# Optimization experiments

Measured on AMD Instinct MI355X. Metric: run time of the kernel, lower is better.

The kernel has to match this reference:

```python
import jax, jax.numpy as jnp
import numpy as np
import math

B, S, D, H, FF = 4, 1024, 1024, 16, 4096
DK = D // H
EPS = 1e-6


def _gelu(x):
    return 0.5 * x * (1 + jnp.tanh(math.sqrt(2 / math.pi) * (x + 0.044715 * x ** 3)))


def _layernorm(x, g, b):
    # torch LayerNorm clone: unbiased std, divide by (std + eps)
    mean = jnp.mean(x, axis=-1, keepdims=True)
    var = jnp.sum((x - mean) ** 2, axis=-1, keepdims=True) / (x.shape[-1] - 1)
    std = jnp.sqrt(var)
    return g * (x - mean) / (std + EPS) + b


def setup_inputs() -> dict:
    key = jax.random.key(0)
    ks = jax.random.split(key, 16)
    sc_d = 1.0 / math.sqrt(D)
    sc_ff = 1.0 / math.sqrt(FF)
    inp = {
        "query": jax.random.normal(ks[0], (B, S, D), jnp.float32),
        "key": jax.random.normal(ks[1], (B, S, D), jnp.float32),
        "value": jax.random.normal(ks[2], (B, S, D), jnp.float32),
        "mask": jnp.ones((B, S), jnp.int32),
        "Wq": jax.random.normal(ks[3], (D, D), jnp.float32) * sc_d,
        "bq": jnp.zeros((D,), jnp.float32),
        "Wk": jax.random.normal(ks[4], (D, D), jnp.float32) * sc_d,
        "bk": jnp.zeros((D,), jnp.float32),
        "Wv": jax.random.normal(ks[5], (D, D), jnp.float32) * sc_d,
        "bv": jnp.zeros((D,), jnp.float32),
        "Wo": jax.random.normal(ks[6], (D, D), jnp.float32) * sc_d,
        "bo": jnp.zeros((D,), jnp.float32),
        "W1": jax.random.normal(ks[7], (FF, D), jnp.float32) * sc_d,
        "b1": jnp.zeros((FF,), jnp.float32),
        "W2": jax.random.normal(ks[8], (D, FF), jnp.float32) * sc_ff,
        "b2": jnp.zeros((D,), jnp.float32),
        "g1": jnp.ones((D,), jnp.float32),
        "be1": jnp.zeros((D,), jnp.float32),
        "g2": jnp.ones((D,), jnp.float32),
        "be2": jnp.zeros((D,), jnp.float32),
    }
    return inp


def reference(query, key, value, mask, Wq, bq, Wk, bk, Wv, bv, Wo, bo,
              W1, b1, W2, b2, g1, be1, g2, be2):
    # self-attention: q = k = v = query (with_external=False)
    def proj(x, W, b):
        return (x @ W.T + b).reshape(B, S, H, DK).transpose(0, 2, 1, 3)  # [B,H,S,DK]

    q = proj(query, Wq, bq)
    k = proj(query, Wk, bk)
    v = proj(query, Wv, bv)
    scores = jnp.einsum("bhqd,bhkd->bhqk", q, k) / math.sqrt(DK)
    # 2D mask [B,S] broadcasts as [B,1,1,S] over key positions
    scores = jnp.where(mask[:, None, None, :] == 0, -1e9, scores)
    p = jax.nn.softmax(scores, axis=-1)
    attn = jnp.einsum("bhqk,bhkd->bhqd", p, v)
    attn = attn.transpose(0, 2, 1, 3).reshape(B, S, D)
    x = attn @ Wo.T + bo
    x = _layernorm(query + x, g1, be1)
    residual = x
    h1 = x @ W1.T + b1
    x2 = _gelu(h1 @ W2.T + b2)  # note: gelu applied AFTER fc2, per source
    return _layernorm(residual + x2, g2, be2)
```

## Files before the change

### kernel.cpp

```cpp
#include <hip/hip_runtime.h>
#include <hip/hip_bf16.h>
#include <math.h>

typedef __bf16 bf16;
typedef __bf16 bf16x8 __attribute__((ext_vector_type(8)));
typedef float floatx4 __attribute__((ext_vector_type(4)));

#define NT 4096
#define DMODEL 1024
#define NHEAD 16
#define DHEAD 64
#define FFDIM 4096

__device__ __forceinline__ void load_lds16(const void* g, void* l) {
    __builtin_amdgcn_global_load_lds(
        (const __attribute__((address_space(1))) void*)g,
        (__attribute__((address_space(3))) void*)l,
        16, 0, 0);
}

__device__ __forceinline__ unsigned short f2bf(float f) {
    bf16 h = (bf16)f;
    return __builtin_bit_cast(unsigned short, h);
}

__device__ __forceinline__ float gelu_f(float v) {
    return 0.5f * v * (1.0f + tanhf(0.7978845608028654f * (v + 0.044715f * v * v * v)));
}

__global__ __launch_bounds__(256) void cast_kernel(
    const float* __restrict__ q, const float* __restrict__ wq, const float* __restrict__ wk,
    const float* __restrict__ wv, const float* __restrict__ wo, const float* __restrict__ w1,
    const float* __restrict__ w2, const float* __restrict__ bq, const float* __restrict__ bk,
    const float* __restrict__ bv, bf16* __restrict__ xbf, bf16* __restrict__ wqkv,
    bf16* __restrict__ wob, bf16* __restrict__ w1b, bf16* __restrict__ w2b,
    float* __restrict__ bqkv)
{
    int gid = blockIdx.x * 256 + threadIdx.x;
    if (gid < 3072)
        bqkv[gid] = gid < 1024 ? bq[gid] : (gid < 2048 ? bk[gid - 1024] : bv[gid - 2048]);

    const float4* src;
    ushort4* dst;
    int off = gid;
    if (off < 1048576)                  { src = (const float4*)q;  dst = (ushort4*)xbf; }
    else if ((off -= 1048576) < 262144) { src = (const float4*)wq; dst = (ushort4*)wqkv; }
    else if ((off -= 262144) < 262144)  { src = (const float4*)wk; dst = (ushort4*)wqkv + 262144; }
    else if ((off -= 262144) < 262144)  { src = (const float4*)wv; dst = (ushort4*)wqkv + 524288; }
    else if ((off -= 262144) < 262144)  { src = (const float4*)wo; dst = (ushort4*)wob; }
    else if ((off -= 262144) < 1048576) { src = (const float4*)w1; dst = (ushort4*)w1b; }
    else { off -= 1048576;                src = (const float4*)w2; dst = (ushort4*)w2b; }

    float4 v = src[off];
    ushort4 u;
    u.x = f2bf(v.x); u.y = f2bf(v.y); u.z = f2bf(v.z); u.w = f2bf(v.w);
    dst[off] = u;
}

template <int EPI, int TN, int SPLITK = 1>
__global__ __launch_bounds__(256) void gemm_bt(
    const bf16* __restrict__ A, const bf16* __restrict__ Wt,
    const float* __restrict__ bias, const float* __restrict__ res,
    void* __restrict__ outp, int M, int N, int K)
{
    constexpr int NJ = TN / 32;
    __shared__ __align__(16) bf16 As[128 * 64];
    __shared__ __align__(16) bf16 Bs[TN * 64];

    const int t = threadIdx.x;
    const int lane = t & 63, wave = t >> 6;
    const int l15 = lane & 15, quad = lane >> 4;
    const int wm = wave & 1, wn = wave >> 1;
    const int m0 = blockIdx.x * 128, n0 = blockIdx.y * TN;
    const int kz = (SPLITK > 1) ? blockIdx.z : 0;
    const int kspan = K / SPLITK;
    const int kstart = kz * kspan;

    floatx4 acc[4][NJ] = {};

    auto issue_loads = [&](int k0) {
        #pragma unroll
        for (int i = 0; i < 4; ++i) {
            int l = t + i * 256;
            int row = l >> 3, ch = (l & 7) ^ (row & 7);
            load_lds16(A + (size_t)(m0 + row) * K + k0 + ch * 8,
                       &As[(size_t)(i * 256 + wave * 64) * 8]);
        }
        #pragma unroll
        for (int i = 0; i < TN / 32; ++i) {
            int l = t + i * 256;
            int row = l >> 3, ch = (l & 7) ^ (row & 7);
            load_lds16(Wt + (size_t)(n0 + row) * K + k0 + ch * 8,
                       &Bs[(size_t)(i * 256 + wave * 64) * 8]);
        }
    };

    const int nk = kspan >> 6;
    issue_loads(kstart);

    for (int it = 0; it < nk; ++it) {
        __syncthreads();

        bf16x8 af[2][4], bfr[2][NJ];
        #pragma unroll
        for (int ks = 0; ks < 2; ++ks) {
            #pragma unroll
            for (int i = 0; i < 4; ++i) {
                int row = wm * 64 + i * 16 + l15;
                int pc = (ks * 4 + quad) ^ (row & 7);
                af[ks][i] = *(const bf16x8*)&As[row * 64 + pc * 8];
            }
            #pragma unroll
            for (int j = 0; j < NJ; ++j) {
                int row = wn * (TN / 2) + j * 16 + l15;
                int pc = (ks * 4 + quad) ^ (row & 7);
                bfr[ks][j] = *(const bf16x8*)&Bs[row * 64 + pc * 8];
            }
        }

        __syncthreads();

        if (it + 1 < nk) issue_loads(kstart + ((it + 1) << 6));

        #pragma unroll
        for (int ks = 0; ks < 2; ++ks)
            #pragma unroll
            for (int i = 0; i < 4; ++i)
                #pragma unroll
                for (int j = 0; j < NJ; ++j)
                    acc[i][j] = __builtin_amdgcn_mfma_f32_16x16x32_bf16(af[ks][i], bfr[ks][j], acc[i][j], 0, 0, 0);
    }

    const int mbase = m0 + wm * 64, nbase = n0 + wn * (TN / 2);
    float* po = (float*)outp + (size_t)kz * ((size_t)M * N);
    #pragma unroll
    for (int i = 0; i < 4; ++i) {
        #pragma unroll
        for (int j = 0; j < NJ; ++j) {
            int col = nbase + j * 16 + l15;
            float bv = (EPI == 3) ? 0.f : bias[col];
            #pragma unroll
            for (int r = 0; r < 4; ++r) {
                int row = mbase + i * 16 + quad * 4 + r;
                size_t idx = (size_t)row * N + col;
                float v = acc[i][j][r] + bv;
                if (EPI == 0) {
                    ((bf16*)outp)[idx] = (bf16)v;
                } else if (EPI == 1) {
                    ((float*)outp)[idx] = v + res[idx];
                } else if (EPI == 2) {
                    ((float*)outp)[idx] = res[idx] + gelu_f(v);
                } else {
                    po[idx] = v;
                }
            }
        }
    }
}

__global__ __launch_bounds__(256) void transpose_v(const bf16* __restrict__ qkv,
                                                   bf16* __restrict__ vt)
{
    __shared__ bf16 tile[64 * 65];
    const int t = threadIdx.x;
    const int bh = blockIdx.y, bb = bh >> 4, h = bh & 15;
    const int s0 = blockIdx.x * 64;

    #pragma unroll
    for (int i = 0; i < 2; ++i) {
        int l = t + i * 256;
        int sl = l >> 3, c = (l & 7) * 8;
        bf16x8 v = *(const bf16x8*)(qkv + (size_t)(bb * 1024 + s0 + sl) * 3072 + 2048 + h * 64 + c);
        #pragma unroll
        for (int j = 0; j < 8; ++j) tile[sl * 65 + c + j] = v[j];
    }
    __syncthreads();
    #pragma unroll
    for (int i = 0; i < 2; ++i) {
        int l = t + i * 256;
        int dl = l >> 3, sc = (l & 7) * 8;
        bf16x8 v;
        #pragma unroll
        for (int j = 0; j < 8; ++j) v[j] = tile[(sc + j) * 65 + dl];
        *(bf16x8*)(vt + (size_t)(bh * 64 + dl) * 1024 + s0 + sc) = v;
    }
}

__global__ __launch_bounds__(256, 4) void flash_attn(
    const bf16* __restrict__ QKV, const bf16* __restrict__ VT,
    const int* __restrict__ mask, bf16* __restrict__ outp)
{
    __shared__ __align__(16) bf16 Ks[2][64 * 64];
    __shared__ __align__(16) bf16 VTs[2][64 * 64];

    const int t = threadIdx.x;
    const int lane = t & 63, wave = t >> 6;
    const int l15 = lane & 15, quad = lane >> 4;
    const int bh = blockIdx.x, bb = bh >> 4, h = bh & 15;
    const int q0 = blockIdx.y * 64;

    #pragma unroll
    for (int i = 0; i < 2; ++i) {
        int l = t + i * 256;
        int row = l >> 3, c = (l & 7) ^ (row & 7);
        load_lds16(QKV + (size_t)(bb * 1024 + q0 + row) * 3072 + h * 64 + c * 8,
                   &VTs[1][(size_t)(i * 256 + wave * 64) * 8]);
    }
    __syncthreads();

    bf16x8 aq[2];
    #pragma unroll
    for (int ks = 0; ks < 2; ++ks) {
        int row = wave * 16 + l15;
        int pc = (ks * 4 + quad) ^ (row & 7);
        aq[ks] = *(const bf16x8*)&VTs[1][row * 64 + pc * 8];
    }
    __syncthreads();

    auto stage_kv = [&](int buf, int kt) {
        #pragma unroll
        for (int i = 0; i < 2; ++i) {
            int l = t + i * 256;
            int row = l >> 3, c = (l & 7) ^ (row & 7);
            int gr = (row & 32) | ((row & 12) << 1) | ((row & 16) >> 2) | (row & 3);
            load_lds16(QKV + (size_t)(bb * 1024 + kt + gr) * 3072 + 1024 + h * 64 + c * 8,
                       &Ks[buf][(size_t)(i * 256 + wave * 64) * 8]);
            load_lds16(VT + (size_t)(bh * 64 + row) * 1024 + kt + c * 8,
                       &VTs[buf][(size_t)(i * 256 + wave * 64) * 8]);
        }
    };
    stage_kv(0, 0);

    floatx4 acc_o[4] = {};
    float m_st = -1e30f, l_st = 0.f;
    const float SC2 = 0.18033688011112042f;
    const float MB  = -1.442695e9f;
    const int* mrow = mask + bb * 1024;

    for (int kt = 0; kt < 1024; kt += 64) {
        const int buf = (kt >> 6) & 1;
        __syncthreads();
        if (kt + 64 < 1024) stage_kv(buf ^ 1, kt + 64);

        int mv = mrow[kt + lane];

        bf16x8 kf[2][4];
        #pragma unroll
        for (int ks = 0; ks < 2; ++ks)
            #pragma unroll
            for (int nt = 0; nt < 4; ++nt) {
                int row = nt * 16 + l15;
                int pc = (ks * 4 + quad) ^ (row & 7);
                kf[ks][nt] = *(const bf16x8*)&Ks[buf][row * 64 + pc * 8];
            }

        floatx4 s[4] = {};
        #pragma unroll
        for (int ks = 0; ks < 2; ++ks)
            #pragma unroll
            for (int nt = 0; nt < 4; ++nt)
                s[nt] = __builtin_amdgcn_mfma_f32_16x16x32_bf16(kf[ks][nt], aq[ks], s[nt], 0, 0, 0);

        bf16x8 vf[2][4];
        #pragma unroll
        for (int ks = 0; ks < 2; ++ks)
            #pragma unroll
            for (int nt2 = 0; nt2 < 4; ++nt2) {
                int row = nt2 * 16 + l15;
                int pc = (ks * 4 + quad) ^ (row & 7);
                vf[ks][nt2] = *(const bf16x8*)&VTs[buf][row * 64 + pc * 8];
            }

        float sv[4][4];
        if (__all(mv != 0)) {
            #pragma unroll
            for (int nt = 0; nt < 4; ++nt)
                #pragma unroll
                for (int r = 0; r < 4; ++r)
                    sv[nt][r] = s[nt][r] * SC2;
        } else {
            #pragma unroll
            for (int nt = 0; nt < 4; ++nt)
                #pragma unroll
                for (int r = 0; r < 4; ++r) {
                    int kg = ((nt >> 1) << 5) | (quad << 3) | ((nt & 1) << 2) | r;
                    int mk = __shfl(mv, kg, 64);
                    sv[nt][r] = fmaf(s[nt][r], SC2, mk ? 0.f : MB);
                }
        }

        float mx = sv[0][0];
        #pragma unroll
        for (int nt = 0; nt < 4; ++nt)
            #pragma unroll
            for (int r = 0; r < 4; ++r)
                mx = fmaxf(mx, sv[nt][r]);
        mx = fmaxf(mx, __shfl_xor(mx, 16, 64));
        mx = fmaxf(mx, __shfl_xor(mx, 32, 64));

        if (__any(mx > m_st + 12.0f)) {
            float mnew = fmaxf(m_st, mx);
            float al = __builtin_amdgcn_exp2f(m_st - mnew);
            m_st = mnew;
            l_st *= al;
            #pragma unroll
            for (int r = 0; r < 4; ++r) {
                float alr = __shfl(al, quad * 4 + r, 64);
                #pragma unroll
                for (int nt2 = 0; nt2 < 4; ++nt2) acc_o[nt2][r] *= alr;
            }
        }

        bf16x8 pa[2];
        float rs = 0.f;
        #pragma unroll
        for (int nt = 0; nt < 4; ++nt)
            #pragma unroll
            for (int r = 0; r < 4; ++r) {
                float p = __builtin_amdgcn_exp2f(sv[nt][r] - m_st);
                rs += p;
                pa[nt >> 1][(nt & 1) * 4 + r] = (bf16)p;
            }
        l_st += rs;

        #pragma unroll
        for (int ks = 0; ks < 2; ++ks)
            #pragma unroll
            for (int nt2 = 0; nt2 < 4; ++nt2)
                acc_o[nt2] = __builtin_amdgcn_mfma_f32_16x16x32_bf16(pa[ks], vf[ks][nt2], acc_o[nt2], 0, 0, 0);
    }

    float lt = l_st;
    lt += __shfl_xor(lt, 16, 64);
    lt += __shfl_xor(lt, 32, 64);
    #pragma unroll
    for (int r = 0; r < 4; ++r) {
        float lr = __shfl(lt, quad * 4 + r, 64);
        float linv = __builtin_amdgcn_rcpf(lr);
        int qrow = q0 + wave * 16 + quad * 4 + r;
        #pragma unroll
        for (int nt2 = 0; nt2 < 4; ++nt2) {
            int dd = nt2 * 16 + l15;
            outp[(size_t)(bb * 1024 + qrow) * 1024 + h * 64 + dd] = (bf16)(acc_o[nt2][r] * linv);
        }
    }
}

template <int MODE>
__global__ __launch_bounds__(256) void ln_fuse(
    const float* __restrict__ part, const float* __restrict__ res,
    const float* __restrict__ bias, const float* __restrict__ g,
    const float* __restrict__ b, bf16* __restrict__ obf, float* __restrict__ of)
{
    const int row = blockIdx.x;
    const size_t base = (size_t)row * 1024;
    float4 p0 = ((const float4*)(part + base))[threadIdx.x];
    float4 p1 = ((const float4*)(part + 4194304 + base))[threadIdx.x];
    float4 rv = ((const float4*)(res + base))[threadIdx.x];
    float4 bi = ((const float4*)bias)[threadIdx.x];
    float4 v;
    if (MODE == 0) {
        v.x = rv.x + p0.x + p1.x + bi.x;
        v.y = rv.y + p0.y + p1.y + bi.y;
        v.z = rv.z + p0.z + p1.z + bi.z;
        v.w = rv.w + p0.w + p1.w + bi.w;
    } else {
        v.x = rv.x + gelu_f(p0.x + p1.x + bi.x);
        v.y = rv.y + gelu_f(p0.y + p1.y + bi.y);
        v.z = rv.z + gelu_f(p0.z + p1.z + bi.z);
        v.w = rv.w + gelu_f(p0.w + p1.w + bi.w);
    }

    float s = v.x + v.y + v.z + v.w;
    float s2 = v.x * v.x + v.y * v.y + v.z * v.z + v.w * v.w;
    #pragma unroll
    for (int o = 32; o >= 1; o >>= 1) {
        s += __shfl_down(s, o, 64);
        s2 += __shfl_down(s2, o, 64);
    }
    __shared__ float red[8];
    if ((threadIdx.x & 63) == 0) {
        red[threadIdx.x >> 6] = s;
        red[4 + (threadIdx.x >> 6)] = s2;
    }
    __syncthreads();
    s = red[0] + red[1] + red[2] + red[3];
    s2 = red[4] + red[5] + red[6] + red[7];
    float mean = s * (1.f / 1024.f);
    float var = fmaxf(0.f, s2 - 1024.f * mean * mean) * (1.f / 1023.f);
    float inv = 1.f / (sqrtf(var) + 1e-6f);
    float4 gg = ((const float4*)g)[threadIdx.x];
    float4 bb = ((const float4*)b)[threadIdx.x];
    float4 o;
    o.x = gg.x * (v.x - mean) * inv + bb.x;
    o.y = gg.y * (v.y - mean) * inv + bb.y;
    o.z = gg.z * (v.z - mean) * inv + bb.z;
    o.w = gg.w * (v.w - mean) * inv + bb.w;
    if (of) ((float4*)(of + base))[threadIdx.x] = o;
    if (obf) {
        ushort4 u;
        u.x = f2bf(o.x); u.y = f2bf(o.y); u.z = f2bf(o.z); u.w = f2bf(o.w);
        ((ushort4*)(obf + base))[threadIdx.x] = u;
    }
}

constexpr size_t OFF_XBF   = 0;
constexpr size_t OFF_WQKV  = OFF_XBF + 8388608;
constexpr size_t OFF_BQKV  = OFF_WQKV + 6291456;
constexpr size_t OFF_WO    = OFF_BQKV + 16384;
constexpr size_t OFF_W1    = OFF_WO + 2097152;
constexpr size_t OFF_W2    = OFF_W1 + 8388608;
constexpr size_t OFF_QKV   = OFF_W2 + 8388608;
constexpr size_t OFF_VT    = OFF_QKV + 25165824;
constexpr size_t OFF_PART  = OFF_QKV;
constexpr size_t OFF_X1BF  = OFF_VT + 8388608;
constexpr size_t OFF_X1F   = OFF_X1BF + 8388608;
constexpr size_t OFF_H1    = OFF_X1F + 16777216;

extern "C" void kernel_launch(void* const* d_in, const int* in_sizes, int n_in,
                              void* d_out, int out_size, void* d_ws, size_t ws_size,
                              hipStream_t stream)
{
    const float* query = (const float*)d_in[0];
    const int*   maskp = (const int*)d_in[3];
    const float* Wq = (const float*)d_in[4];
    const float* bq = (const float*)d_in[5];
    const float* Wk = (const float*)d_in[6];
    const float* bk = (const float*)d_in[7];
    const float* Wv = (const float*)d_in[8];
    const float* bv = (const float*)d_in[9];
    const float* Wo = (const float*)d_in[10];
    const float* bo = (const float*)d_in[11];
    const float* W1 = (const float*)d_in[12];
    const float* b1 = (const float*)d_in[13];
    const float* W2 = (const float*)d_in[14];
    const float* b2 = (const float*)d_in[15];
    const float* g1 = (const float*)d_in[16];
    const float* be1 = (const float*)d_in[17];
    const float* g2 = (const float*)d_in[18];
    const float* be2 = (const float*)d_in[19];

    char* ws = (char*)d_ws;
    bf16*  xbf   = (bf16*)(ws + OFF_XBF);
    bf16*  wqkv  = (bf16*)(ws + OFF_WQKV);
    float* bqkv  = (float*)(ws + OFF_BQKV);
    bf16*  wob   = (bf16*)(ws + OFF_WO);
    bf16*  w1b   = (bf16*)(ws + OFF_W1);
    bf16*  w2b   = (bf16*)(ws + OFF_W2);
    bf16*  qkv   = (bf16*)(ws + OFF_QKV);
    bf16*  vt    = (bf16*)(ws + OFF_VT);
    float* part  = (float*)(ws + OFF_PART);
    bf16*  x1bf  = (bf16*)(ws + OFF_X1BF);
    float* x1f   = (float*)(ws + OFF_X1F);
    bf16*  h1    = (bf16*)(ws + OFF_H1);
    bf16*  attn  = (bf16*)(ws + OFF_XBF);
    float* outf  = (float*)d_out;

    cast_kernel<<<16384, 256, 0, stream>>>(query, Wq, Wk, Wv, Wo, W1, W2, bq, bk, bv,
                                           xbf, wqkv, wob, w1b, w2b, bqkv);
    gemm_bt<0, 128><<<dim3(32, 24), 256, 0, stream>>>(xbf, wqkv, bqkv, nullptr, qkv, NT, 3072, 1024);
    transpose_v<<<dim3(16, 64), 256, 0, stream>>>(qkv, vt);
    flash_attn<<<dim3(64, 16), 256, 0, stream>>>(qkv, vt, maskp, attn);
    gemm_bt<3, 128, 2><<<dim3(32, 8, 2), 256, 0, stream>>>(attn, wob, nullptr, nullptr, part, NT, 1024, 1024);
    ln_fuse<0><<<4096, 256, 0, stream>>>(part, query, bo, g1, be1, x1bf, x1f);
    gemm_bt<0, 128><<<dim3(32, 32), 256, 0, stream>>>(x1bf, w1b, b1, nullptr, h1, NT, 4096, 1024);
    gemm_bt<3, 128, 2><<<dim3(32, 8, 2), 256, 0, stream>>>(h1, w2b, nullptr, nullptr, part, NT, 1024, 4096);
    ln_fuse<1><<<4096, 256, 0, stream>>>(part, x1f, b2, g2, be2, nullptr, outf);
}
```

Baseline: 331.2 us.

## Add 256x256 multi-buffered 8-wave GEMM for QKV, FC1 and FC2 with split-K 4

Adds a new GEMM kernel with 256x256 tiles, 512 threads, a 4-stage LDS ring fed by direct global-to-LDS loads, swizzled LDS layout, and priority hints around the MFMA bursts. It replaces the 128-tile GEMM for the QKV projection, FC1 and FC2. FC2 switches to split-K 4 written to a new partial buffer, and the layernorm kernel is generalized to sum NP partials. The larger tiles aim to raise arithmetic intensity and improve overlap of loads with MFMA. The cost is more register and LDS pressure, fewer blocks per GEMM (192 to 256), and extra partial-sum traffic for FC2.

```diff
diff --git a/kernel.cpp b/kernel.cpp
--- a/kernel.cpp
+++ b/kernel.cpp
@@ -55,6 +55,125 @@
     ushort4 u;
     u.x = f2bf(v.x); u.y = f2bf(v.y); u.z = f2bf(v.z); u.w = f2bf(v.w);
     dst[off] = u;
+}
+
+template <int EPI, int SPLITK = 1>
+__global__ __launch_bounds__(512, 2) void gemm8(
+    const bf16* __restrict__ A, const bf16* __restrict__ Wt,
+    const float* __restrict__ bias, void* __restrict__ outp,
+    int M, int N, int K)
+{
+    __shared__ __align__(16) bf16 As[4][256 * 32];
+    __shared__ __align__(16) bf16 Bs[4][256 * 32];
+
+    const int t = threadIdx.x;
+    const int lane = t & 63, wave = t >> 6;
+    const int l15 = lane & 15, quad = lane >> 4;
+    const int wm = wave >> 2, wn = wave & 3;
+    const int m0 = blockIdx.x * 256, n0 = blockIdx.y * 256;
+    const int kz = (SPLITK > 1) ? blockIdx.z : 0;
+    const int kspan = K / SPLITK, kstart = kz * kspan;
+    const int nk = kspan >> 5;
+
+    floatx4 acc[8][4] = {};
+
+    auto stageA = [&](int T) {
+        int b = T & 3, k0 = kstart + T * 32;
+        #pragma unroll
+        for (int i = 0; i < 2; ++i) {
+            int l = t + i * 512;
+            int row = l >> 2, ch = (l & 3) ^ ((row >> 1) & 3);
+            load_lds16(A + (size_t)(m0 + row) * K + k0 + ch * 8,
+                       &As[b][(size_t)(i * 512 + wave * 64) * 8]);
+        }
+    };
+    auto stageB = [&](int T) {
+        int b = T & 3, k0 = kstart + T * 32;
+        #pragma unroll
+        for (int i = 0; i < 2; ++i) {
+            int l = t + i * 512;
+            int row = l >> 2, ch = (l & 3) ^ ((row >> 1) & 3);
+            load_lds16(Wt + (size_t)(n0 + row) * K + k0 + ch * 8,
+                       &Bs[b][(size_t)(i * 512 + wave * 64) * 8]);
+        }
+    };
+
+    stageA(0); stageB(0); stageA(1); stageB(1); stageA(2); stageB(2);
+    asm volatile("s_waitcnt vmcnt(8)" ::: "memory");
+    __builtin_amdgcn_s_barrier();
+    __builtin_amdgcn_sched_barrier(0);
+
+    for (int T = 0; T < nk; ++T) {
+        const int b = T & 3;
+        bf16x8 af[4], bfr[4];
+
+        #pragma unroll
+        for (int i = 0; i < 4; ++i) {
+            int ra = wm * 128 + i * 16 + l15;
+            af[i]  = *(const bf16x8*)&As[b][ra * 32 + (quad ^ ((ra >> 1) & 3)) * 8];
+            int rb = wn * 64 + i * 16 + l15;
+            bfr[i] = *(const bf16x8*)&Bs[b][rb * 32 + (quad ^ ((rb >> 1) & 3)) * 8];
+        }
+        if (T + 3 < nk) stageA(T + 3);
+        __builtin_amdgcn_s_setprio(1);
+        #pragma unroll
+        for (int i = 0; i < 4; ++i)
+            #pragma unroll
+            for (int j = 0; j < 4; ++j)
+                acc[i][j] = __builtin_amdgcn_mfma_f32_16x16x32_bf16(af[i], bfr[j], acc[i][j], 0, 0, 0);
+        __builtin_amdgcn_s_setprio(0);
+
+        #pragma unroll
+        for (int i = 0; i < 4; ++i) {
+            int ra = wm * 128 + (i + 4) * 16 + l15;
+            af[i] = *(const bf16x8*)&As[b][ra * 32 + (quad ^ ((ra >> 1) & 3)) * 8];
+        }
+        if (T + 3 < nk) stageB(T + 3);
+        __builtin_amdgcn_s_setprio(1);
+        #pragma unroll
+        for (int i = 0; i < 4; ++i)
+            #pragma unroll
+            for (int j = 0; j < 4; ++j)
+                acc[i + 4][j] = __builtin_amdgcn_mfma_f32_16x16x32_bf16(af[i], bfr[j], acc[i + 4][j], 0, 0, 0);
+        __builtin_amdgcn_s_setprio(0);
+
+        if (T + 1 < nk) {
+            if (T + 3 < nk)       asm volatile("s_waitcnt vmcnt(8)" ::: "memory");
+            else if (T + 3 == nk) asm volatile("s_waitcnt vmcnt(4)" ::: "memory");
+            else                  asm volatile("s_waitcnt vmcnt(0)" ::: "memory");
+            __builtin_amdgcn_s_barrier();
+            __builtin_amdgcn_sched_barrier(0);
+        }
+    }
+
+    const int mbase = m0 + wm * 128, nbase = n0 + wn * 64;
+    if (EPI == 0) {
+        #pragma unroll
+        for (int j = 0; j < 4; ++j) {
+            int col = nbase + j * 16 + l15;
+            float bv = bias[col];
+            #pragma unroll
+            for (int i = 0; i < 8; ++i)
+                #pragma unroll
+                for (int r = 0; r < 4; ++r) {
+                    int row = mbase + i * 16 + quad * 4 + r;
+                    ((bf16*)outp)[(size_t)row * N + col] = (bf16)(acc[i][j][r] + bv);
+                }
+        }
+    } else {
+        float* po = (float*)outp + (size_t)kz * ((size_t)M * N);
+        #pragma unroll
+        for (int j = 0; j < 4; ++j) {
+            int col = nbase + j * 16 + l15;
+            #pragma unroll
+            for (int i = 0; i < 8; ++i)
+                #pragma unroll
+                for (int r = 0; r < 4; ++r) {
+                    int row = mbase + i * 16 + quad * 4 + r;
+                    po[(size_t)row * N + col] = acc[i][j][r];
+                }
+        }
+    }
 }
 
 template <int EPI, int TN, int SPLITK = 1>
@@ -346,7 +465,7 @@
     }
 }
 
-template <int MODE>
+template <int MODE, int NP>
 __global__ __launch_bounds__(256) void ln_fuse(
     const float* __restrict__ part, const float* __restrict__ res,
     const float* __restrict__ bias, const float* __restrict__ g,
@@ -354,21 +473,25 @@
 {
     const int row = blockIdx.x;
     const size_t base = (size_t)row * 1024;
-    float4 p0 = ((const float4*)(part + base))[threadIdx.x];
-    float4 p1 = ((const float4*)(part + 4194304 + base))[threadIdx.x];
+    float4 p = {0.f, 0.f, 0.f, 0.f};
+    #pragma unroll
+    for (int k = 0; k < NP; ++k) {
+        float4 pk = ((const float4*)(part + (size_t)k * 4194304 + base))[threadIdx.x];
+        p.x += pk.x; p.y += pk.y; p.z += pk.z; p.w += pk.w;
+    }
     float4 rv = ((const float4*)(res + base))[threadIdx.x];
     float4 bi = ((const float4*)bias)[threadIdx.x];
     float4 v;
     if (MODE == 0) {
-        v.x = rv.x + p0.x + p1.x + bi.x;
-        v.y = rv.y + p0.y + p1.y + bi.y;
-        v.z = rv.z + p0.z + p1.z + bi.z;
-        v.w = rv.w + p0.w + p1.w + bi.w;
+        v.x = rv.x + p.x + bi.x;
+        v.y = rv.y + p.y + bi.y;
+        v.z = rv.z + p.z + bi.z;
+        v.w = rv.w + p.w + bi.w;
     } else {
-        v.x = rv.x + gelu_f(p0.x + p1.x + bi.x);
-        v.y = rv.y + gelu_f(p0.y + p1.y + bi.y);
-        v.z = rv.z + gelu_f(p0.z + p1.z + bi.z);
-        v.w = rv.w + gelu_f(p0.w + p1.w + bi.w);
+        v.x = rv.x + gelu_f(p.x + bi.x);
+        v.y = rv.y + gelu_f(p.y + bi.y);
+        v.z = rv.z + gelu_f(p.z + bi.z);
+        v.w = rv.w + gelu_f(p.w + bi.w);
     }
 
     float s = v.x + v.y + v.z + v.w;
@@ -412,10 +535,11 @@
 constexpr size_t OFF_W2    = OFF_W1 + 8388608;
 constexpr size_t OFF_QKV   = OFF_W2 + 8388608;
 constexpr size_t OFF_VT    = OFF_QKV + 25165824;
-constexpr size_t OFF_PART  = OFF_QKV;
+constexpr size_t OFF_PARTO = OFF_QKV;
 constexpr size_t OFF_X1BF  = OFF_VT + 8388608;
 constexpr size_t OFF_X1F   = OFF_X1BF + 8388608;
 constexpr size_t OFF_H1    = OFF_X1F + 16777216;
+constexpr size_t OFF_PARTF = OFF_H1 + 33554432;
 
 extern "C" void kernel_launch(void* const* d_in, const int* in_sizes, int n_in,
                               void* d_out, int out_size, void* d_ws, size_t ws_size,
@@ -449,21 +573,22 @@
     bf16*  w2b   = (bf16*)(ws + OFF_W2);
     bf16*  qkv   = (bf16*)(ws + OFF_QKV);
     bf16*  vt    = (bf16*)(ws + OFF_VT);
-    float* part  = (float*)(ws + OFF_PART);
+    float* partO = (float*)(ws + OFF_PARTO);
     bf16*  x1bf  = (bf16*)(ws + OFF_X1BF);
     float* x1f   = (float*)(ws + OFF_X1F);
     bf16*  h1    = (bf16*)(ws + OFF_H1);
+    float* partF = (float*)(ws + OFF_PARTF);
     bf16*  attn  = (bf16*)(ws + OFF_XBF);
     float* outf  = (float*)d_out;
 
     cast_kernel<<<16384, 256, 0, stream>>>(query, Wq, Wk, Wv, Wo, W1, W2, bq, bk, bv,
                                            xbf, wqkv, wob, w1b, w2b, bqkv);
-    gemm_bt<0, 128><<<dim3(32, 24), 256, 0, stream>>>(xbf, wqkv, bqkv, nullptr, qkv, NT, 3072, 1024);
+    gemm8<0><<<dim3(16, 12), 512, 0, stream>>>(xbf, wqkv, bqkv, qkv, NT, 3072, 1024);
     transpose_v<<<dim3(16, 64), 256, 0, stream>>>(qkv, vt);
     flash_attn<<<dim3(64, 16), 256, 0, stream>>>(qkv, vt, maskp, attn);
-    gemm_bt<3, 128, 2><<<dim3(32, 8, 2), 256, 0, stream>>>(attn, wob, nullptr, nullptr, part, NT, 1024, 1024);
-    ln_fuse<0><<<4096, 256, 0, stream>>>(part, query, bo, g1, be1, x1bf, x1f);
-    gemm_bt<0, 128><<<dim3(32, 32), 256, 0, stream>>>(x1bf, w1b, b1, nullptr, h1, NT, 4096, 1024);
-    gemm_bt<3, 128, 2><<<dim3(32, 8, 2), 256, 0, stream>>>(h1, w2b, nullptr, nullptr, part, NT, 1024, 4096);
-    ln_fuse<1><<<4096, 256, 0, stream>>>(part, x1f, b2, g2, be2, nullptr, outf);
-}
+    gemm_bt<3, 128, 2><<<dim3(32, 8, 2), 256, 0, stream>>>(attn, wob, nullptr, nullptr, partO, NT, 1024, 1024);
+    ln_fuse<0, 2><<<4096, 256, 0, stream>>>(partO, query, bo, g1, be1, x1bf, x1f);
+    gemm8<0><<<dim3(16, 16), 512, 0, stream>>>(x1bf, w1b, b1, h1, NT, 4096, 1024);
+    gemm8<3, 4><<<dim3(16, 4, 4), 512, 0, stream>>>(h1, w2b, nullptr, partF, NT, 1024, 4096);
+    ln_fuse<1, 4><<<4096, 256, 0, stream>>>(partF, x1f, b2, g2, be2, nullptr, outf);
+}
```

Result: slower. 364.4 us (+10.0%).
